# Performance work log

Measured on AMD Instinct MI355X. Metric: run time of the kernel, lower is better.

## Reference

```python
import jax, jax.numpy as jnp
import numpy as np

K = 98          # fixed_n_tokens
HEADS = 8
EPS = 1e-5      # BatchNorm eps


def setup_inputs() -> dict:
    key = jax.random.key(0)
    ks = jax.random.split(key, 8)
    B, C, H, W = 32, 384, 56, 56

    def p(k, shape, scale=0.02):
        return jax.random.normal(k, shape, jnp.float32) * scale

    return {
        "x": jax.random.normal(ks[0], (B, C, H, W), jnp.float32),
        "qkv_w": p(ks[1], (3 * C, C)),
        "qkv_b": jnp.zeros((3 * C,), jnp.float32),
        "proj_w": p(ks[2], (C, C)),
        "proj_b": jnp.zeros((C,), jnp.float32),
        "bn_g": jnp.ones((C,), jnp.float32),
        "bn_b": jnp.zeros((C,), jnp.float32),
        "fc1_w": p(ks[3], (C, C)),
        "fc1_b": jnp.zeros((C,), jnp.float32),
        "fc2_w": p(ks[4], (C, C)),
        "fc2_b": jnp.zeros((C,), jnp.float32),
        "dw_w": p(ks[5], (C, 1, 3, 3), 0.1),  # depthwise 3x3, groups=C
        "dw_b": jnp.zeros((C,), jnp.float32),
    }


def reference(x, qkv_w, qkv_b, proj_w, proj_b, bn_g, bn_b,
              fc1_w, fc1_b, fc2_w, fc2_b, dw_w, dw_b):
    B, C, H, W = x.shape
    N = H * W
    head_dim = C // HEADS
    scale = head_dim ** -0.5

    # ---- salience top-k selection (pool_size=(1,1): no pooling) ----
    xf = x.reshape(B, C, N)
    scores = jnp.sum(xf * xf, axis=1)                       # [B, N]
    _, top_idx = jax.lax.top_k(scores, K)                   # [B, K]
    top = jnp.take_along_axis(xf, top_idx[:, None, :], axis=2)   # [B, C, K]
    bg = (xf.sum(2) - top.sum(2)) / (N - K)                 # [B, C]
    tokens = jnp.concatenate([top, bg[:, :, None]], axis=2)      # [B, C, K+1]
    tokens = tokens.transpose(0, 2, 1)                      # [B, K+1, C]

    # ---- tiny attention over K+1 tokens ----
    n = K + 1
    qkv = tokens @ qkv_w.T + qkv_b                          # [B, n, 3C]
    qkv = qkv.reshape(B, n, 3, HEADS, head_dim).transpose(2, 0, 3, 1, 4)
    q, k, v = qkv[0], qkv[1], qkv[2]                        # [B, h, n, d]
    attn = jax.nn.softmax(scale * jnp.einsum('bhnd,bhmd->bhnm', q, k), axis=-1)
    res = jnp.einsum('bhnm,bhmd->bhnd', attn, v)            # [B, h, n, d]
    attn_out = res.transpose(0, 1, 3, 2).reshape(B, C, n)   # b (h d) n

    # ---- scatter-restore: bg token everywhere, top tokens at their slots ----
    top_res, bg_res = attn_out[:, :, :K], attn_out[:, :, K:]    # [B,C,K], [B,C,1]
    restored = jnp.broadcast_to(bg_res, (B, C, N))
    bi = jnp.arange(B)[:, None, None]
    ci = jnp.arange(C)[None, :, None]
    restored = restored.at[bi, ci, top_idx[:, None, :]].set(top_res)
    restored = restored.reshape(B, C, H, W)  # interpolate is identity (same size)

    # ---- conv branch: BN (batch stats) -> fc1 -> gelu -> dwconv -> fc2 ----
    mu = x.mean(axis=(0, 2, 3), keepdims=True)
    var = x.var(axis=(0, 2, 3), keepdims=True)
    xn = (x - mu) * jax.lax.rsqrt(var + EPS)
    xn = xn * bn_g[None, :, None, None] + bn_b[None, :, None, None]
    h1 = jnp.einsum('bchw,oc->bohw', xn, fc1_w) + fc1_b[None, :, None, None]
    h1 = jax.nn.gelu(h1, approximate=False)
    h2 = jax.lax.conv_general_dilated(
        h1, dw_w, window_strides=(1, 1), padding='SAME',
        dimension_numbers=('NCHW', 'OIHW', 'NCHW'), feature_group_count=C)
    h2 = h2 + dw_b[None, :, None, None]
    conv_out = jnp.einsum('bchw,oc->bohw', h2, fc2_w) + fc2_b[None, :, None, None]

    combined = restored + conv_out
    return jnp.einsum('bchw,oc->bohw', combined, proj_w) + proj_b[None, :, None, None]
```

## Files before the change

kernel.cpp:

```cpp
#include <hip/hip_runtime.h>
#include <hip/hip_bf16.h>
#include <math.h>

typedef unsigned short u16;
typedef short short8 __attribute__((ext_vector_type(8)));
typedef float floatx4 __attribute__((ext_vector_type(4)));

#define B_    32
#define C_    384
#define N_    3136
#define K_TOP 98
#define NTOK  99
#define TOKS  (B_ * NTOK)
#define HEADS_ 8
#define HD    48
#define KDIM  384

__device__ __forceinline__ float b2f(u16 u) {
    unsigned int x = ((unsigned int)u) << 16;
    return __builtin_bit_cast(float, x);
}
__device__ __forceinline__ u16 f2b(float f) {
    unsigned int x = __builtin_bit_cast(unsigned int, f);
    unsigned int r = (x + 0x7fffu + ((x >> 16) & 1u)) >> 16;
    return (u16)r;
}
__device__ __forceinline__ u16 tob16(float f) { return f2b(f); }
__device__ __forceinline__ u16 tob16(u16 u) { return u; }


__global__ void k_zero(float* sumsq) { sumsq[threadIdx.x] = 0.f; }

__global__ void k_cvt(const float* __restrict__ src, u16* __restrict__ dst, int n) {
    int i = blockIdx.x * 256 + threadIdx.x;
    if (i < n) dst[i] = f2b(src[i]);
}

__global__ void k_scores(const float* __restrict__ x, float* __restrict__ scores) {
    int gid = blockIdx.x * 256 + threadIdx.x;
    int b = gid / N_;
    int p = gid - b * N_;
    const float* xp = x + (size_t)b * C_ * N_ + p;
    float s = 0.f;
#pragma unroll 8
    for (int c = 0; c < C_; ++c) {
        float v = xp[(size_t)c * N_];
        s += v * v;
    }
    scores[gid] = s;
}

__global__ void k_chsum(const float* __restrict__ x, float* __restrict__ ch_sum,
                        float* __restrict__ sumsq) {
    int bc = blockIdx.x;
    int c = bc % C_;
    const float* xp = x + (size_t)bc * N_;
    float s1 = 0.f, s2 = 0.f;
    for (int p = threadIdx.x; p < N_; p += 256) {
        float v = xp[p];
        s1 += v; s2 += v * v;
    }
#pragma unroll
    for (int off = 32; off; off >>= 1) {
        s1 += __shfl_down(s1, off);
        s2 += __shfl_down(s2, off);
    }
    __shared__ float r1[4], r2[4];
    int wave = threadIdx.x >> 6;
    if ((threadIdx.x & 63) == 0) { r1[wave] = s1; r2[wave] = s2; }
    __syncthreads();
    if (threadIdx.x == 0) {
        float a = r1[0] + r1[1] + r1[2] + r1[3];
        float b2 = r2[0] + r2[1] + r2[2] + r2[3];
        ch_sum[bc] = a;
        atomicAdd(&sumsq[c], b2);
    }
}

__launch_bounds__(1024)
__global__ void k_topk(const float* __restrict__ scores, int* __restrict__ idx,
                       int* __restrict__ istop) {
    int b = blockIdx.x;
    int tid = threadIdx.x;
    __shared__ unsigned int keys[N_];
    __shared__ int hist[4096];
    __shared__ unsigned int sh_prefix;
    __shared__ int sh_g;
    __shared__ int c1, tc;
    __shared__ int idxbuf[K_TOP];
    __shared__ int tiebuf[128];

    for (int p = tid; p < N_; p += 1024) {
        keys[p] = __builtin_bit_cast(unsigned int, scores[b * N_ + p]);
        istop[b * N_ + p] = 0;
    }

    int Kcur = K_TOP;
    unsigned int prefix = 0;
    int m = 0;
#pragma unroll
    for (int pass = 0; pass < 3; ++pass) {
        const int shift = (pass == 0) ? 20 : (pass == 1 ? 8 : 0);
        const int nbins = (pass == 2) ? 256 : 4096;
        const unsigned int pm = (pass == 0) ? 0u : (pass == 1 ? 0xFFF00000u : 0xFFFFFF00u);
        for (int i = tid; i < nbins; i += 1024) hist[i] = 0;
        __syncthreads();
        for (int p = tid; p < N_; p += 1024) {
            unsigned int u = keys[p];
            if ((u & pm) == prefix) atomicAdd(&hist[(u >> shift) & (nbins - 1)], 1);
        }
        __syncthreads();
        if (tid < 64) {
            int lane = tid;
            int nch = nbins >> 6;
            int s = 0;
            for (int j = 0; j < nch; ++j) s += hist[lane * nch + j];
            int suf = s;
#pragma unroll
            for (int off = 1; off < 64; off <<= 1) {
                int v = __shfl_down(suf, off);
                if (lane + off < 64) suf += v;
            }
            int above = suf - s;
            if (suf >= Kcur && above < Kcur) {
                int acc = above;
                int bin = (lane + 1) * nch - 1;
                for (;; --bin) {
                    int h = hist[bin];
                    if (acc + h >= Kcur) break;
                    acc += h;
                }
                sh_prefix = prefix | ((unsigned int)bin << shift);
                sh_g = acc;
            }
        }
        __syncthreads();
        prefix = sh_prefix;
        m += sh_g;
        Kcur -= sh_g;
    }

    unsigned int lo = prefix;
    if (tid == 0) { c1 = 0; tc = 0; }
    __syncthreads();
    for (int p = tid; p < N_; p += 1024) {
        unsigned int u = keys[p];
        if (u > lo) { int pos = atomicAdd(&c1, 1); idxbuf[pos] = p; }
        else if (u == lo) { int pos = atomicAdd(&tc, 1); if (pos < 128) tiebuf[pos] = p; }
    }
    __syncthreads();
    if (tid == 0) {
        int need = K_TOP - m;
        if (tc <= 128) {
            int cnt = tc;
            for (int r = 0; r < need; ++r) {
                int mi = r;
                for (int q = r + 1; q < cnt; ++q) if (tiebuf[q] < tiebuf[mi]) mi = q;
                int t = tiebuf[mi]; tiebuf[mi] = tiebuf[r]; tiebuf[r] = t;
                idxbuf[m + r] = t;
            }
        } else {
            int picked = 0;
            for (int p = 0; p < N_ && picked < need; ++p)
                if (keys[p] == lo) { idxbuf[m + picked] = p; ++picked; }
        }
    }
    __syncthreads();
    if (tid < K_TOP) {
        int ib = idxbuf[tid];
        idx[b * K_TOP + tid] = ib;
        istop[b * N_ + ib] = tid + 1;
    }
}

__launch_bounds__(256)
__global__ void k_tokens(const float* __restrict__ x, const int* __restrict__ idx,
                         const float* __restrict__ ch_sum, u16* __restrict__ tokensT) {
    int b = blockIdx.x, cg = blockIdx.y;
    __shared__ int il[K_TOP];
    int tid = threadIdx.x;
    if (tid < K_TOP) il[tid] = idx[b * K_TOP + tid];
    __syncthreads();
    int cl = tid >> 2;
    int js = tid & 3;
    int c = cg * 64 + cl;
    const float* xp = x + (size_t)b * C_ * N_ + (size_t)c * N_;
    u16* tp = tokensT + (size_t)c * TOKS + b * NTOK;
    float s = 0.f;
    for (int j = js; j < K_TOP; j += 4) {
        float v = xp[il[j]];
        tp[j] = f2b(v);
        s += v;
    }
    s += __shfl_down(s, 2);
    s += __shfl_down(s, 1);
    if (js == 0) {
        float bg = (ch_sum[b * C_ + c] - s) * (1.0f / (float)(N_ - K_TOP));
        tp[K_TOP] = f2b(bg);
    }
}

__global__ void k_bnfin(const float* ch_sum, const float* sumsq, const float* bn_g,
                        const float* bn_b, float* a_scale, float* b_shift) {
    int c = threadIdx.x;
    float s = 0.f;
    for (int b = 0; b < B_; ++b) s += ch_sum[b * C_ + c];
    float inv_n = 1.0f / (float)(B_ * N_);
    float mu = s * inv_n;
    float var = sumsq[c] * inv_n - mu * mu;
    float a = rsqrtf(var + 1e-5f) * bn_g[c];
    a_scale[c] = a;
    b_shift[c] = bn_b[c] - mu * a;
}

__global__ void k_bias2p(const float* __restrict__ fc2_w, const float* __restrict__ fc2_b,
                         const float* __restrict__ dw_b, float* __restrict__ bias2p) {
    int c = blockIdx.x * 4 + (threadIdx.x >> 6);
    int l = threadIdx.x & 63;
    float acc = 0.f;
    for (int k = l; k < C_; k += 64) acc += fc2_w[c * C_ + k] * dw_b[k];
#pragma unroll
    for (int off = 32; off; off >>= 1) acc += __shfl_down(acc, off);
    if (l == 0) bias2p[c] = acc + fc2_b[c];
}

__global__ void k_biasM(const float* __restrict__ proj_w, const float* __restrict__ proj_b,
                        const float* __restrict__ bias2p, float* __restrict__ biasM) {
    int o = blockIdx.x * 4 + (threadIdx.x >> 6);
    int l = threadIdx.x & 63;
    float acc = 0.f;
    for (int c = l; c < C_; c += 64) acc += proj_w[o * C_ + c] * bias2p[c];
#pragma unroll
    for (int off = 32; off; off >>= 1) acc += __shfl_down(acc, off);
    if (l == 0) biasM[o] = acc + proj_b[o];
}

__global__ void k_bias1(const float* __restrict__ fc1_w, const float* __restrict__ fc1_b,
                        const float* __restrict__ b_shift, float* __restrict__ bias1) {
    int o = blockIdx.x * 4 + (threadIdx.x >> 6);
    int l = threadIdx.x & 63;
    float acc = 0.f;
    for (int c = l; c < C_; c += 64) acc += fc1_w[o * C_ + c] * b_shift[c];
#pragma unroll
    for (int off = 32; off; off >>= 1) acc += __shfl_down(acc, off);
    if (l == 0) bias1[o] = acc + fc1_b[o];
}

__global__ void k_cbias(const float* __restrict__ proj_w, const float* __restrict__ biasM,
                        const float* __restrict__ bgres, float* __restrict__ cbias) {
    int b = blockIdx.y;
    int o = blockIdx.x * 4 + (threadIdx.x >> 6);
    int l = threadIdx.x & 63;
    float acc = 0.f;
    for (int c = l; c < C_; c += 64) acc += proj_w[o * C_ + c] * bgres[b * C_ + c];
#pragma unroll
    for (int off = 32; off; off >>= 1) acc += __shfl_down(acc, off);
    if (l == 0) cbias[b * C_ + o] = acc + biasM[o];
}

__global__ void k_mw(const float* __restrict__ proj_w, const float* __restrict__ fc2_w,
                     u16* __restrict__ Mw) {
    int o = blockIdx.x, c = threadIdx.x;
    float acc = 0.f;
    for (int k = 0; k < C_; ++k) acc += proj_w[o * C_ + k] * fc2_w[k * C_ + c];
    Mw[o * C_ + c] = f2b(acc);
}

__global__ void k_w1p(const float* fc1_w, const float* a_scale, u16* W1p) {
    int i = blockIdx.x * 256 + threadIdx.x;
    if (i < C_ * C_) {
        int c = i % C_;
        W1p[i] = f2b(fc1_w[i] * a_scale[c]);
    }
}

__launch_bounds__(256)
__global__ void k_gemm_qkv(const u16* __restrict__ A, const u16* __restrict__ Bsrc,
                           const float* __restrict__ biasB, float* __restrict__ outF) {
    const int ldB = TOKS, NC = TOKS;
    int m0 = blockIdx.x * 128;
    int n0 = blockIdx.y * 64;
    int tid = threadIdx.x;
    int lane = tid & 63;
    int wave = tid >> 6;
    int wm0 = (wave >> 1) * 64;
    int wn0 = (wave & 1) * 32;
    int lm = lane & 15;
    int quad = lane >> 4;

    __shared__ __attribute__((aligned(16))) u16 Al[128 * 32];
    __shared__ __attribute__((aligned(16))) u16 Bl[64 * 32];

    floatx4 acc[4][2];
#pragma unroll
    for (int i = 0; i < 4; ++i)
#pragma unroll
        for (int j = 0; j < 2; ++j)
#pragma unroll
            for (int r = 0; r < 4; ++r) acc[i][j][r] = 0.f;

    int ar = tid >> 2;
    int akc = (tid & 3) * 8;
    int bp = tid & 63;
    int bgi = tid >> 6;
    int bswz = ((bgi ^ ((bp >> 1) & 3)) & 3) * 8;
    int bcol = n0 + bp;
    bool bok = bcol < NC;

    for (int kt = 0; kt < 12; ++kt) {
        int k0 = kt * 32;
        __syncthreads();
#pragma unroll
        for (int i = 0; i < 2; ++i) {
            int r = ar + i * 64;
            short8 v = *(const short8*)(const void*)(A + (size_t)(m0 + r) * KDIM + k0 + akc);
            *(short8*)(void*)&Al[r * 32 + akc] = v;
        }
        {
            const u16* src = Bsrc + (size_t)(k0 + bgi * 8) * ldB + bcol;
            short8 v;
#pragma unroll
            for (int j = 0; j < 8; ++j)
                v[j] = bok ? (short)src[(size_t)j * ldB] : (short)0;
            *(short8*)(void*)&Bl[bp * 32 + bswz] = v;
        }
        __syncthreads();
        short8 af[4], bfv[2];
#pragma unroll
        for (int mt = 0; mt < 4; ++mt)
            af[mt] = *(const short8*)(const void*)&Al[(wm0 + mt * 16 + lm) * 32 + quad * 8];
#pragma unroll
        for (int nt = 0; nt < 2; ++nt) {
            int prow = wn0 + nt * 16 + lm;
            int sw = ((quad ^ ((prow >> 1) & 3)) & 3) * 8;
            bfv[nt] = *(const short8*)(const void*)&Bl[prow * 32 + sw];
        }
#pragma unroll
        for (int mt = 0; mt < 4; ++mt)
#pragma unroll
            for (int nt = 0; nt < 2; ++nt)
                acc[mt][nt] = __builtin_amdgcn_mfma_f32_16x16x32_bf16(af[mt], bfv[nt], acc[mt][nt], 0, 0, 0);
    }

#pragma unroll
    for (int nt = 0; nt < 2; ++nt) {
        int col = n0 + wn0 + nt * 16 + lm;
        if (col >= NC) continue;
#pragma unroll
        for (int mt = 0; mt < 4; ++mt)
#pragma unroll
            for (int r = 0; r < 4; ++r) {
                int o = m0 + wm0 + mt * 16 + quad * 4 + r;
                outF[(size_t)o * TOKS + col] = acc[mt][nt][r] + biasB[o];
            }
    }
}

template<int MODE, typename TB>
__launch_bounds__(512, 4)
__global__ void k_gemm2(const u16* __restrict__ A, const TB* __restrict__ B0, long bStride,
                        const float* __restrict__ biasF,
                        float* __restrict__ outF,
                        u16* __restrict__ outB,
                        const float* __restrict__ cbias, const int* __restrict__ istop,
                        const float* __restrict__ delta2) {
    const int ldB = N_;
    int b = blockIdx.y;
    int n0 = blockIdx.x * 64;
    const TB* Bsrc = B0 + (long)b * bStride;
    int tid = threadIdx.x;
    int lane = tid & 63;
    int wave = tid >> 6;
    int wm0 = wave * 48;
    int lm = lane & 15;
    int quad = lane >> 4;

    __shared__ __attribute__((aligned(16))) u16 Bl[2][64 * 96];

    int col = lane;
    int gcol = n0 + col;
    int swzc = (col >> 1) & 3;
    u16* lp = &Bl[0][col * 96 + wave];

    floatx4 acc[3][4];
#pragma unroll
    for (int i = 0; i < 3; ++i)
#pragma unroll
        for (int j = 0; j < 4; ++j)
#pragma unroll
            for (int r = 0; r < 4; ++r) acc[i][j][r] = 0.f;

    TB rv[12];
    {
        const TB* sp = Bsrc + (size_t)wave * ldB + gcol;
#pragma unroll
        for (int i = 0; i < 12; ++i) rv[i] = sp[(size_t)(8 * i) * ldB];
#pragma unroll
        for (int i = 0; i < 12; ++i)
            lp[(i >> 2) * 32 + (((i & 3) ^ swzc) & 3) * 8] = tob16(rv[i]);
    }
    __syncthreads();

    for (int ch = 0; ch < 4; ++ch) {
        int cur = ch & 1;
        if (ch < 3) {
            const TB* sp = Bsrc + (size_t)((ch + 1) * 96 + wave) * ldB + gcol;
#pragma unroll
            for (int i = 0; i < 12; ++i) rv[i] = sp[(size_t)(8 * i) * ldB];
        }
#pragma unroll
        for (int kt = 0; kt < 3; ++kt) {
            int k0 = ch * 96 + kt * 32;
            short8 af[3], bfv[4];
#pragma unroll
            for (int mt = 0; mt < 3; ++mt)
                af[mt] = *(const short8*)(const void*)(A + (size_t)(wm0 + mt * 16 + lm) * KDIM + k0 + quad * 8);
#pragma unroll
            for (int nt = 0; nt < 4; ++nt) {
                int pc = nt * 16 + lm;
                int sw = ((quad ^ ((pc >> 1) & 3)) & 3) * 8;
                bfv[nt] = *(const short8*)(const void*)&Bl[cur][pc * 96 + kt * 32 + sw];
            }
#pragma unroll
            for (int mt = 0; mt < 3; ++mt)
#pragma unroll
                for (int nt = 0; nt < 4; ++nt)
                    acc[mt][nt] = __builtin_amdgcn_mfma_f32_16x16x32_bf16(af[mt], bfv[nt], acc[mt][nt], 0, 0, 0);
        }
        if (ch < 3) {
            u16* wp = lp + (cur ^ 1) * (64 * 96);
#pragma unroll
            for (int i = 0; i < 12; ++i)
                wp[(i >> 2) * 32 + (((i & 3) ^ swzc) & 3) * 8] = tob16(rv[i]);
            __syncthreads();
        }
    }

#pragma unroll
    for (int nt = 0; nt < 4; ++nt) {
        int ocol = n0 + nt * 16 + lm;
        int tt = 0;
        if (MODE == 3) tt = istop[b * N_ + ocol];
#pragma unroll
        for (int mt = 0; mt < 3; ++mt) {
#pragma unroll
            for (int r = 0; r < 4; ++r) {
                int o = wm0 + mt * 16 + quad * 4 + r;
                float val = acc[mt][nt][r];
                if (MODE == 2) {
                    outF[(size_t)o * N_ + ocol] = val;
                } else if (MODE == 1) {
                    val += biasF[o];
                    float g = 0.5f * val * (1.0f + erff(val * 0.70710678118654752f));
                    outB[(size_t)b * C_ * N_ + (size_t)o * N_ + ocol] = f2b(g);
                } else {
                    val += cbias[b * C_ + o];
                    if (tt) val += delta2[(size_t)o * N_ + b * K_TOP + (tt - 1)];
                    outF[(size_t)b * C_ * N_ + (size_t)o * N_ + ocol] = val;
                }
            }
        }
    }
}


__global__ void k_attn_scores(const float* __restrict__ qkv, float* __restrict__ Sws) {
    int b = blockIdx.x, h = blockIdx.y;
    __shared__ float ql[NTOK * HD], kl[NTOK * HD];
    int tid = threadIdx.x;
    const float scale = 0.14433756729740643f;
    for (int u = tid; u < NTOK * HD; u += 256) {
        int d = u / NTOK, j = u - d * NTOK;
        size_t base = (size_t)(h * HD + d) * TOKS + b * NTOK + j;
        ql[j * HD + d] = qkv[base] * scale;
        kl[j * HD + d] = qkv[base + (size_t)C_ * TOKS];
    }
    __syncthreads();
    float* Sp = Sws + (size_t)(b * HEADS_ + h) * (NTOK * NTOK);
    for (int u = tid; u < NTOK * NTOK; u += 256) {
        int i = u / NTOK, j = u - i * NTOK;
        float s = 0.f;
#pragma unroll 8
        for (int d = 0; d < HD; ++d) s += ql[i * HD + d] * kl[j * HD + d];
        Sp[u] = s;
    }
}

__global__ void k_attn_out(const float* __restrict__ qkv, const float* __restrict__ Sws,
                           u16* __restrict__ diffT, float* __restrict__ bgres) {
    int b = blockIdx.x, h = blockIdx.y;
    __shared__ float vl[NTOK * HD];
    __shared__ float P[NTOK * 100];
    __shared__ float bgrow[HD];
    int tid = threadIdx.x;
    for (int u = tid; u < NTOK * HD; u += 256) {
        int d = u / NTOK, j = u - d * NTOK;
        vl[j * HD + d] = qkv[(size_t)(2 * C_ + h * HD + d) * TOKS + b * NTOK + j];
    }
    __syncthreads();
    const float* Sp = Sws + (size_t)(b * HEADS_ + h) * (NTOK * NTOK);
    if (tid < NTOK) {
        int i = tid;
        float mx = -1e30f;
        for (int j = 0; j < NTOK; ++j) mx = fmaxf(mx, Sp[i * NTOK + j]);
        float sum = 0.f;
        for (int j = 0; j < NTOK; ++j) { float e = expf(Sp[i * NTOK + j] - mx); P[i * 100 + j] = e; sum += e; }
        float inv = 1.f / sum;
        for (int j = 0; j < NTOK; ++j) P[i * 100 + j] *= inv;
    }
    __syncthreads();
    if (tid < HD) {
        int d = tid;
        float a = 0.f;
        for (int j = 0; j < NTOK; ++j) a += P[K_TOP * 100 + j] * vl[j * HD + d];
        bgrow[d] = a;
        bgres[b * C_ + h * HD + d] = a;
    }
    __syncthreads();
    for (int u = tid; u < K_TOP * HD; u += 256) {
        int d = u / K_TOP, i = u - d * K_TOP;
        float a = 0.f;
        for (int j = 0; j < NTOK; ++j) a += P[i * 100 + j] * vl[j * HD + d];
        diffT[(size_t)(h * HD + d) * N_ + b * K_TOP + i] = f2b(a - bgrow[d]);
    }
}

__launch_bounds__(256)
__global__ void k_dwconv(u16* __restrict__ h1, const float* __restrict__ dw_w) {
    int bc = blockIdx.x;
    int c = bc % C_;
    __shared__ __attribute__((aligned(16))) u16 tile[4256];
    int tid = threadIdx.x;
#pragma unroll
    for (int i = tid; i < 532; i += 256)
        *(short8*)(void*)&tile[i * 8] = (short8)0;
    float w[9];
#pragma unroll
    for (int t = 0; t < 9; ++t) w[t] = dw_w[c * 9 + t];
    __syncthreads();
    u16* src = h1 + (size_t)bc * N_;
    for (int i = tid; i < 392; i += 256) {
        int y = i / 7, xg = i - y * 7;
        short8 v = *(const short8*)(const void*)(src + i * 8);
        *(short8*)(void*)&tile[(y + 2) * 72 + xg * 8] = v;
    }
    __syncthreads();
    for (int g = tid; g < 392; g += 256) {
        int y = g / 7, xg = (g - y * 7) * 8;
        float out[8];
#pragma unroll
        for (int t = 0; t < 8; ++t) out[t] = 0.f;
#pragma unroll
        for (int ky = 0; ky < 3; ++ky) {
            const u16* rp = &tile[(y + ky + 1) * 72 + xg];
            short8 mid = *(const short8*)(const void*)rp;
            float r[10];
            r[0] = b2f(rp[-1]);
#pragma unroll
            for (int t = 0; t < 8; ++t) r[t + 1] = b2f((u16)mid[t]);
            r[9] = b2f(rp[8]);
#pragma unroll
            for (int kx = 0; kx < 3; ++kx) {
                float wv = w[ky * 3 + kx];
#pragma unroll
                for (int t = 0; t < 8; ++t) out[t] += wv * r[t + kx];
            }
        }
        short8 o;
#pragma unroll
        for (int t = 0; t < 8; ++t) o[t] = (short)f2b(out[t]);
        *(short8*)(void*)(src + g * 8) = o;
    }
}


extern "C" void kernel_launch(void* const* d_in, const int* in_sizes, int n_in,
                              void* d_out, int out_size, void* d_ws, size_t ws_size,
                              hipStream_t stream) {
    (void)in_sizes; (void)n_in; (void)out_size; (void)ws_size;
    const float* x      = (const float*)d_in[0];
    const float* qkv_w  = (const float*)d_in[1];
    const float* qkv_b  = (const float*)d_in[2];
    const float* proj_w = (const float*)d_in[3];
    const float* proj_b = (const float*)d_in[4];
    const float* bn_g   = (const float*)d_in[5];
    const float* bn_b   = (const float*)d_in[6];
    const float* fc1_w  = (const float*)d_in[7];
    const float* fc1_b  = (const float*)d_in[8];
    const float* fc2_w  = (const float*)d_in[9];
    const float* fc2_b  = (const float*)d_in[10];
    const float* dw_w   = (const float*)d_in[11];
    const float* dw_b   = (const float*)d_in[12];
    float* out = (float*)d_out;

    float* qkvF = (float*)d_out;
    float* Sws  = (float*)((char*)d_out + (size_t)3 * C_ * TOKS * 4);

    char* w = (char*)d_ws;
    constexpr size_t o_h1      = 0;
    constexpr size_t o_scores  = o_h1      + (size_t)B_ * C_ * N_ * 2;
    constexpr size_t o_chsum   = o_scores  + (size_t)B_ * N_ * 4;
    constexpr size_t o_sumsq   = o_chsum   + (size_t)B_ * C_ * 4;
    constexpr size_t o_idx     = o_sumsq   + (size_t)C_ * 4;
    constexpr size_t o_istop   = o_idx     + (size_t)B_ * K_TOP * 4;
    constexpr size_t o_tokens  = o_istop   + (size_t)B_ * N_ * 4;
    constexpr size_t o_ascale  = o_tokens  + (size_t)C_ * TOKS * 2;
    constexpr size_t o_bshift  = o_ascale  + (size_t)C_ * 4;
    constexpr size_t o_w1p     = o_bshift  + (size_t)C_ * 4;
    constexpr size_t o_bias1   = o_w1p     + (size_t)C_ * C_ * 2;
    constexpr size_t o_mw      = o_bias1   + (size_t)C_ * 4;
    constexpr size_t o_biasM   = o_mw      + (size_t)C_ * C_ * 2;
    constexpr size_t o_bias2p  = o_biasM   + (size_t)C_ * 4;
    constexpr size_t o_cbias   = o_bias2p  + (size_t)C_ * 4;
    constexpr size_t o_bgres   = o_cbias   + (size_t)B_ * C_ * 4;
    constexpr size_t o_difft   = o_bgres   + (size_t)B_ * C_ * 4;
    constexpr size_t o_delta2  = o_difft   + (size_t)C_ * N_ * 2;
    constexpr size_t o_wq16    = o_delta2  + (size_t)C_ * N_ * 4;
    constexpr size_t o_pw16    = o_wq16    + (size_t)3 * C_ * C_ * 2;

    u16*   h1      = (u16*)(w + o_h1);
    float* scores  = (float*)(w + o_scores);
    float* ch_sum  = (float*)(w + o_chsum);
    float* sumsq   = (float*)(w + o_sumsq);
    int*   idx     = (int*)(w + o_idx);
    int*   istop   = (int*)(w + o_istop);
    u16*   tokensT = (u16*)(w + o_tokens);
    float* a_scale = (float*)(w + o_ascale);
    float* b_shift = (float*)(w + o_bshift);
    u16*   W1p     = (u16*)(w + o_w1p);
    float* bias1   = (float*)(w + o_bias1);
    u16*   Mw      = (u16*)(w + o_mw);
    float* biasM   = (float*)(w + o_biasM);
    float* bias2p  = (float*)(w + o_bias2p);
    float* cbias   = (float*)(w + o_cbias);
    float* bgres   = (float*)(w + o_bgres);
    u16*   diffT   = (u16*)(w + o_difft);
    float* Delta2  = (float*)(w + o_delta2);
    u16*   Wq16    = (u16*)(w + o_wq16);
    u16*   Pw16    = (u16*)(w + o_pw16);

    k_zero<<<1, C_, 0, stream>>>(sumsq);
    k_scores<<<(B_ * N_) / 256, 256, 0, stream>>>(x, scores);
    k_chsum<<<B_ * C_, 256, 0, stream>>>(x, ch_sum, sumsq);
    k_topk<<<B_, 1024, 0, stream>>>(scores, idx, istop);
    k_tokens<<<dim3(B_, 6), 256, 0, stream>>>(x, idx, ch_sum, tokensT);
    k_bnfin<<<1, C_, 0, stream>>>(ch_sum, sumsq, bn_g, bn_b, a_scale, b_shift);
    k_bias2p<<<96, 256, 0, stream>>>(fc2_w, fc2_b, dw_b, bias2p);
    k_mw<<<C_, C_, 0, stream>>>(proj_w, fc2_w, Mw);
    k_biasM<<<96, 256, 0, stream>>>(proj_w, proj_b, bias2p, biasM);
    k_w1p<<<(C_ * C_ + 255) / 256, 256, 0, stream>>>(fc1_w, a_scale, W1p);
    k_bias1<<<96, 256, 0, stream>>>(fc1_w, fc1_b, b_shift, bias1);
    k_cvt<<<(3 * C_ * C_ + 255) / 256, 256, 0, stream>>>(qkv_w, Wq16, 3 * C_ * C_);
    k_cvt<<<(C_ * C_ + 255) / 256, 256, 0, stream>>>(proj_w, Pw16, C_ * C_);

    k_gemm_qkv<<<dim3(9, 50), 256, 0, stream>>>(Wq16, tokensT, qkv_b, qkvF);
    k_attn_scores<<<dim3(B_, HEADS_), 256, 0, stream>>>(qkvF, Sws);
    k_attn_out<<<dim3(B_, HEADS_), 256, 0, stream>>>(qkvF, Sws, diffT, bgres);
    k_cbias<<<dim3(96, B_), 256, 0, stream>>>(proj_w, biasM, bgres, cbias);
    k_gemm2<2, u16><<<dim3(49, 1), 512, 0, stream>>>(Pw16, diffT, 0,
        nullptr, Delta2, nullptr, nullptr, nullptr, nullptr);
    k_gemm2<1, float><<<dim3(49, 32), 512, 0, stream>>>(W1p, x, (long)C_ * N_,
        bias1, nullptr, h1, nullptr, nullptr, nullptr);
    k_dwconv<<<B_ * C_, 256, 0, stream>>>(h1, dw_w);
    k_gemm2<3, u16><<<dim3(49, 32), 512, 0, stream>>>(Mw, h1, (long)C_ * N_,
        nullptr, out, nullptr, cbias, istop, Delta2);
}
```

Baseline: 731.1 us.

## Fuse x statistics passes with bf16 conversion and restage GEMM B tiles

Replaces the separate score and channel-sum kernels with one pass over x that computes channel sums, sum of squares and partial per-pixel scores, and also writes a bf16 copy of x. A small kernel then finishes the scores. The fc1 GEMM reads the bf16 copy instead of fp32 x, which halves its input traffic. The shared B tile is reorganised into 128-deep K chunks written as 16-byte vectors with an XOR swizzle. The cost is an extra bf16 write of x, stored in scratch space inside the output buffer at a fixed offset.

After: 849.4 us. +16.2%, slower.

```diff
diff --git a/kernel.cpp b/kernel.cpp
--- a/kernel.cpp
+++ b/kernel.cpp
@@ -25,8 +25,6 @@
     unsigned int r = (x + 0x7fffu + ((x >> 16) & 1u)) >> 16;
     return (u16)r;
 }
-__device__ __forceinline__ u16 tob16(float f) { return f2b(f); }
-__device__ __forceinline__ u16 tob16(u16 u) { return u; }
 
 
 __global__ void k_zero(float* sumsq) { sumsq[threadIdx.x] = 0.f; }
@@ -36,45 +34,67 @@
     if (i < n) dst[i] = f2b(src[i]);
 }
 
-__global__ void k_scores(const float* __restrict__ x, float* __restrict__ scores) {
+__launch_bounds__(256)
+__global__ void k_xprep(const float* __restrict__ x, float* __restrict__ ch_sum,
+                        float* __restrict__ sumsq, float* __restrict__ spart,
+                        u16* __restrict__ xb) {
+    int b = blockIdx.x, cg = blockIdx.y;
+    int c0 = cg * 64;
+    int tid = threadIdx.x;
+    int lane = tid & 63;
+    int wave = tid >> 6;
+    __shared__ float wsum1[64 * 4], wsum2[64 * 4];
+
+    float ps[13];
+#pragma unroll
+    for (int i = 0; i < 13; ++i) ps[i] = 0.f;
+
+    for (int c = 0; c < 64; ++c) {
+        const float* row = x + ((size_t)(b * C_ + c0 + c)) * N_;
+        u16* xrow = xb + ((size_t)(b * C_ + c0 + c)) * N_;
+        float s1 = 0.f, s2 = 0.f;
+#pragma unroll
+        for (int i = 0; i < 13; ++i) {
+            int p = tid + i * 256;
+            if (p < N_) {
+                float v = row[p];
+                xrow[p] = f2b(v);
+                float v2 = v * v;
+                s1 += v; s2 += v2; ps[i] += v2;
+            }
+        }
+#pragma unroll
+        for (int off = 32; off; off >>= 1) {
+            s1 += __shfl_down(s1, off);
+            s2 += __shfl_down(s2, off);
+        }
+        if (lane == 0) { wsum1[c * 4 + wave] = s1; wsum2[c * 4 + wave] = s2; }
+    }
+    float* sp = spart + (size_t)(b * 6 + cg) * N_;
+#pragma unroll
+    for (int i = 0; i < 13; ++i) {
+        int p = tid + i * 256;
+        if (p < N_) sp[p] = ps[i];
+    }
+    __syncthreads();
+    if (tid < 64) {
+        int c = tid;
+        float a = wsum1[c * 4] + wsum1[c * 4 + 1] + wsum1[c * 4 + 2] + wsum1[c * 4 + 3];
+        float q = wsum2[c * 4] + wsum2[c * 4 + 1] + wsum2[c * 4 + 2] + wsum2[c * 4 + 3];
+        ch_sum[b * C_ + c0 + c] = a;
+        atomicAdd(&sumsq[c0 + c], q);
+    }
+}
+
+__global__ void k_scores_fin(const float* __restrict__ spart, float* __restrict__ scores) {
     int gid = blockIdx.x * 256 + threadIdx.x;
     int b = gid / N_;
     int p = gid - b * N_;
-    const float* xp = x + (size_t)b * C_ * N_ + p;
+    const float* sp = spart + (size_t)b * 6 * N_ + p;
     float s = 0.f;
-#pragma unroll 8
-    for (int c = 0; c < C_; ++c) {
-        float v = xp[(size_t)c * N_];
-        s += v * v;
-    }
+#pragma unroll
+    for (int j = 0; j < 6; ++j) s += sp[(size_t)j * N_];
     scores[gid] = s;
-}
-
-__global__ void k_chsum(const float* __restrict__ x, float* __restrict__ ch_sum,
-                        float* __restrict__ sumsq) {
-    int bc = blockIdx.x;
-    int c = bc % C_;
-    const float* xp = x + (size_t)bc * N_;
-    float s1 = 0.f, s2 = 0.f;
-    for (int p = threadIdx.x; p < N_; p += 256) {
-        float v = xp[p];
-        s1 += v; s2 += v * v;
-    }
-#pragma unroll
-    for (int off = 32; off; off >>= 1) {
-        s1 += __shfl_down(s1, off);
-        s2 += __shfl_down(s2, off);
-    }
-    __shared__ float r1[4], r2[4];
-    int wave = threadIdx.x >> 6;
-    if ((threadIdx.x & 63) == 0) { r1[wave] = s1; r2[wave] = s2; }
-    __syncthreads();
-    if (threadIdx.x == 0) {
-        float a = r1[0] + r1[1] + r1[2] + r1[3];
-        float b2 = r2[0] + r2[1] + r2[2] + r2[3];
-        ch_sum[bc] = a;
-        atomicAdd(&sumsq[c], b2);
-    }
 }
 
 __launch_bounds__(1024)
@@ -356,9 +376,9 @@
     }
 }
 
-template<int MODE, typename TB>
+template<int MODE>
 __launch_bounds__(512, 4)
-__global__ void k_gemm2(const u16* __restrict__ A, const TB* __restrict__ B0, long bStride,
+__global__ void k_gemm2(const u16* __restrict__ A, const u16* __restrict__ B0, long bStride,
                         const float* __restrict__ biasF,
                         float* __restrict__ outF,
                         u16* __restrict__ outB,
@@ -367,7 +387,7 @@
     const int ldB = N_;
     int b = blockIdx.y;
     int n0 = blockIdx.x * 64;
-    const TB* Bsrc = B0 + (long)b * bStride;
+    const u16* Bsrc = B0 + (size_t)b * bStride;
     int tid = threadIdx.x;
     int lane = tid & 63;
     int wave = tid >> 6;
@@ -375,12 +395,12 @@
     int lm = lane & 15;
     int quad = lane >> 4;
 
-    __shared__ __attribute__((aligned(16))) u16 Bl[2][64 * 96];
-
-    int col = lane;
-    int gcol = n0 + col;
-    int swzc = (col >> 1) & 3;
-    u16* lp = &Bl[0][col * 96 + wave];
+    __shared__ __attribute__((aligned(16))) u16 Bl[2][64 * 128];
+
+    int sc = tid & 63;
+    int kg = tid >> 6;
+    int w0 = ((kg ^ (sc & 7)) * 8);
+    const u16* bsp = Bsrc + (size_t)n0 + sc;
 
     floatx4 acc[3][4];
 #pragma unroll
@@ -390,27 +410,28 @@
 #pragma unroll
             for (int r = 0; r < 4; ++r) acc[i][j][r] = 0.f;
 
-    TB rv[12];
+    short8 r0, r1;
     {
-        const TB* sp = Bsrc + (size_t)wave * ldB + gcol;
-#pragma unroll
-        for (int i = 0; i < 12; ++i) rv[i] = sp[(size_t)(8 * i) * ldB];
-#pragma unroll
-        for (int i = 0; i < 12; ++i)
-            lp[(i >> 2) * 32 + (((i & 3) ^ swzc) & 3) * 8] = tob16(rv[i]);
-    }
-    __syncthreads();
-
-    for (int ch = 0; ch < 4; ++ch) {
+        const u16* p0 = bsp + (size_t)(kg * 8) * ldB;
+        const u16* p1 = bsp + (size_t)(64 + kg * 8) * ldB;
+#pragma unroll
+        for (int j = 0; j < 8; ++j) { r0[j] = (short)p0[(size_t)j * ldB]; r1[j] = (short)p1[(size_t)j * ldB]; }
+        *(short8*)(void*)&Bl[0][sc * 128 + w0] = r0;
+        *(short8*)(void*)&Bl[0][sc * 128 + 64 + w0] = r1;
+    }
+    __syncthreads();
+
+    for (int ch = 0; ch < 3; ++ch) {
         int cur = ch & 1;
-        if (ch < 3) {
-            const TB* sp = Bsrc + (size_t)((ch + 1) * 96 + wave) * ldB + gcol;
-#pragma unroll
-            for (int i = 0; i < 12; ++i) rv[i] = sp[(size_t)(8 * i) * ldB];
-        }
-#pragma unroll
-        for (int kt = 0; kt < 3; ++kt) {
-            int k0 = ch * 96 + kt * 32;
+        if (ch < 2) {
+            const u16* p0 = bsp + (size_t)((ch + 1) * 128 + kg * 8) * ldB;
+            const u16* p1 = bsp + (size_t)((ch + 1) * 128 + 64 + kg * 8) * ldB;
+#pragma unroll
+            for (int j = 0; j < 8; ++j) { r0[j] = (short)p0[(size_t)j * ldB]; r1[j] = (short)p1[(size_t)j * ldB]; }
+        }
+#pragma unroll
+        for (int kt = 0; kt < 4; ++kt) {
+            int k0 = ch * 128 + kt * 32;
             short8 af[3], bfv[4];
 #pragma unroll
             for (int mt = 0; mt < 3; ++mt)
@@ -418,8 +439,8 @@
 #pragma unroll
             for (int nt = 0; nt < 4; ++nt) {
                 int pc = nt * 16 + lm;
-                int sw = ((quad ^ ((pc >> 1) & 3)) & 3) * 8;
-                bfv[nt] = *(const short8*)(const void*)&Bl[cur][pc * 96 + kt * 32 + sw];
+                int win = kt * 4 + quad;
+                bfv[nt] = *(const short8*)(const void*)&Bl[cur][pc * 128 + ((win ^ (pc & 7)) * 8)];
             }
 #pragma unroll
             for (int mt = 0; mt < 3; ++mt)
@@ -427,11 +448,9 @@
                 for (int nt = 0; nt < 4; ++nt)
                     acc[mt][nt] = __builtin_amdgcn_mfma_f32_16x16x32_bf16(af[mt], bfv[nt], acc[mt][nt], 0, 0, 0);
         }
-        if (ch < 3) {
-            u16* wp = lp + (cur ^ 1) * (64 * 96);
-#pragma unroll
-            for (int i = 0; i < 12; ++i)
-                wp[(i >> 2) * 32 + (((i & 3) ^ swzc) & 3) * 8] = tob16(rv[i]);
+        if (ch < 2) {
+            *(short8*)(void*)&Bl[cur ^ 1][sc * 128 + w0] = r0;
+            *(short8*)(void*)&Bl[cur ^ 1][sc * 128 + 64 + w0] = r1;
             __syncthreads();
         }
     }
@@ -595,6 +614,7 @@
 
     float* qkvF = (float*)d_out;
     float* Sws  = (float*)((char*)d_out + (size_t)3 * C_ * TOKS * 4);
+    u16*   xb   = (u16*)((char*)d_out + (size_t)32 * 1024 * 1024);
 
     char* w = (char*)d_ws;
     constexpr size_t o_h1      = 0;
@@ -617,6 +637,7 @@
     constexpr size_t o_delta2  = o_difft   + (size_t)C_ * N_ * 2;
     constexpr size_t o_wq16    = o_delta2  + (size_t)C_ * N_ * 4;
     constexpr size_t o_pw16    = o_wq16    + (size_t)3 * C_ * C_ * 2;
+    constexpr size_t o_spart   = o_pw16    + (size_t)C_ * C_ * 2;
 
     u16*   h1      = (u16*)(w + o_h1);
     float* scores  = (float*)(w + o_scores);
@@ -638,10 +659,11 @@
     float* Delta2  = (float*)(w + o_delta2);
     u16*   Wq16    = (u16*)(w + o_wq16);
     u16*   Pw16    = (u16*)(w + o_pw16);
+    float* spart   = (float*)(w + o_spart);
 
     k_zero<<<1, C_, 0, stream>>>(sumsq);
-    k_scores<<<(B_ * N_) / 256, 256, 0, stream>>>(x, scores);
-    k_chsum<<<B_ * C_, 256, 0, stream>>>(x, ch_sum, sumsq);
+    k_xprep<<<dim3(B_, 6), 256, 0, stream>>>(x, ch_sum, sumsq, spart, xb);
+    k_scores_fin<<<(B_ * N_) / 256, 256, 0, stream>>>(spart, scores);
     k_topk<<<B_, 1024, 0, stream>>>(scores, idx, istop);
     k_tokens<<<dim3(B_, 6), 256, 0, stream>>>(x, idx, ch_sum, tokensT);
     k_bnfin<<<1, C_, 0, stream>>>(ch_sum, sumsq, bn_g, bn_b, a_scale, b_shift);
@@ -657,11 +679,11 @@
     k_attn_scores<<<dim3(B_, HEADS_), 256, 0, stream>>>(qkvF, Sws);
     k_attn_out<<<dim3(B_, HEADS_), 256, 0, stream>>>(qkvF, Sws, diffT, bgres);
     k_cbias<<<dim3(96, B_), 256, 0, stream>>>(proj_w, biasM, bgres, cbias);
-    k_gemm2<2, u16><<<dim3(49, 1), 512, 0, stream>>>(Pw16, diffT, 0,
+    k_gemm2<2><<<dim3(49, 1), 512, 0, stream>>>(Pw16, diffT, 0,
         nullptr, Delta2, nullptr, nullptr, nullptr, nullptr);
-    k_gemm2<1, float><<<dim3(49, 32), 512, 0, stream>>>(W1p, x, (long)C_ * N_,
+    k_gemm2<1><<<dim3(49, 32), 512, 0, stream>>>(W1p, xb, (long)C_ * N_,
         bias1, nullptr, h1, nullptr, nullptr, nullptr);
     k_dwconv<<<B_ * C_, 256, 0, stream>>>(h1, dw_w);
-    k_gemm2<3, u16><<<dim3(49, 32), 512, 0, stream>>>(Mw, h1, (long)C_ * N_,
+    k_gemm2<3><<<dim3(49, 32), 512, 0, stream>>>(Mw, h1, (long)C_ * N_,
         nullptr, out, nullptr, cbias, istop, Delta2);
 }
```
